# Kernel optimization log

Measured on AMD Instinct MI355X. Metric: run time of the kernel, lower is better.

## Reference

```python
import jax, jax.numpy as jnp
import numpy as np

OVERFLOW_MARGIN = 1e-08

N, D, OUT = 8192, 128, 128


def setup_inputs() -> dict:
    key = jax.random.key(0)
    k1, k2, k3 = jax.random.split(key, 3)
    values = jax.random.normal(k1, (N, D), dtype=jnp.float32)
    adjacency = jax.random.uniform(k2, (N, N), dtype=jnp.float32)
    W = jax.random.normal(k3, (D, OUT), dtype=jnp.float32) * 0.05
    b = jnp.zeros((OUT,), dtype=jnp.float32)
    return {"values": values, "adjacency": adjacency, "W": W, "b": b}


def reference(values, adjacency, W, b):
    # Dense projection: fc_sc = values @ W + b  -> [N, OUT]
    fc_sc = values @ W + b
    # degree d = A @ ones -> row sums, [N]
    d = jnp.sum(adjacency, axis=1)
    d_inv_sqrt = 1.0 / (jnp.sqrt(d) + OVERFLOW_MARGIN)  # [N]
    # laplacian = diag(d_inv_sqrt) @ A @ diag(d_inv_sqrt)
    # expressed as row/col broadcast scaling (same math, no NxN diag matmuls)
    laplacian = adjacency * d_inv_sqrt[:, None] * d_inv_sqrt[None, :]
    # graph conv: [N,N] @ [N,OUT]
    return laplacian @ fc_sc
```

## Files before the change

kernel.cpp:

```cpp
#include <hip/hip_runtime.h>

#define NROWS 8192
#define DIM   128
#define RSTRIDE 136

typedef __attribute__((ext_vector_type(8))) short  short8;
typedef __attribute__((ext_vector_type(4))) float  floatx4;

union frag_u { unsigned u[4]; short8 v; };

__device__ __forceinline__ unsigned pk_bf16(float a, float b) {
  unsigned ua = __float_as_uint(a);
  ua += 0x7fffu + ((ua >> 16) & 1u);
  unsigned ub = __float_as_uint(b);
  ub += 0x7fffu + ((ub >> 16) & 1u);
  return (ua >> 16) | (ub & 0xffff0000u);
}

__global__ __launch_bounds__(256) void k_rowsum(const float* __restrict__ A,
                                                float* __restrict__ s) {
  int row = blockIdx.x;
  const float4* A4 = (const float4*)(A + (size_t)row * NROWS);
  float sum = 0.f;
#pragma unroll
  for (int it = 0; it < NROWS / 4 / 256; ++it) {
    float4 v = A4[threadIdx.x + it * 256];
    sum += (v.x + v.y) + (v.z + v.w);
  }
#pragma unroll
  for (int off = 32; off > 0; off >>= 1) sum += __shfl_down(sum, off, 64);
  __shared__ float red[4];
  int lane = threadIdx.x & 63, w = threadIdx.x >> 6;
  if (lane == 0) red[w] = sum;
  __syncthreads();
  if (threadIdx.x == 0) {
    float d = (red[0] + red[1]) + (red[2] + red[3]);
    s[row] = 1.0f / (sqrtf(d) + 1e-8f);
  }
}

__global__ __launch_bounds__(256) void k_fc(const float* __restrict__ V,
                                            const float* __restrict__ W,
                                            const float* __restrict__ b,
                                            const float* __restrict__ s,
                                            unsigned short* __restrict__ gT) {
  __shared__ float Wl[DIM * DIM];
  __shared__ float Vl[32 * DIM];
  __shared__ unsigned short Fl[32 * DIM];
  int r0 = blockIdx.x * 32;
  {
    const float4* Wg = (const float4*)W;
    float4* Wd = (float4*)Wl;
#pragma unroll
    for (int i = 0; i < DIM * DIM / 4 / 256; ++i)
      Wd[threadIdx.x + i * 256] = Wg[threadIdx.x + i * 256];
    const float4* Vg = (const float4*)(V + (size_t)r0 * DIM);
    float4* Vd = (float4*)Vl;
#pragma unroll
    for (int i = 0; i < 32 * DIM / 4 / 256; ++i)
      Vd[threadIdx.x + i * 256] = Vg[threadIdx.x + i * 256];
  }
  __syncthreads();

  int cg = threadIdx.x & 31;
  int rg = threadIdx.x >> 5;
  float acc[4][4] = {};
  for (int d = 0; d < DIM; ++d) {
    float4 w = *(const float4*)&Wl[d * DIM + cg * 4];
#pragma unroll
    for (int rr = 0; rr < 4; ++rr) {
      float v = Vl[(rg * 4 + rr) * DIM + d];
      acc[rr][0] += v * w.x; acc[rr][1] += v * w.y;
      acc[rr][2] += v * w.z; acc[rr][3] += v * w.w;
    }
  }
  float bb[4], sv[4];
#pragma unroll
  for (int cc = 0; cc < 4; ++cc) bb[cc] = b[cg * 4 + cc];
#pragma unroll
  for (int rr = 0; rr < 4; ++rr) sv[rr] = s[r0 + rg * 4 + rr];
#pragma unroll
  for (int rr = 0; rr < 4; ++rr)
#pragma unroll
    for (int cc = 0; cc < 4; cc += 2) {
      unsigned p = pk_bf16((acc[rr][cc]     + bb[cc])     * sv[rr],
                           (acc[rr][cc + 1] + bb[cc + 1]) * sv[rr]);
      *(unsigned*)&Fl[(rg * 4 + rr) * DIM + cg * 4 + cc] = p;
    }
  __syncthreads();

  int k = threadIdx.x & 127, h = threadIdx.x >> 7;
  unsigned wb[8];
#pragma unroll
  for (int rr = 0; rr < 8; ++rr) {
    unsigned lo = Fl[(h * 16 + 2 * rr) * DIM + k];
    unsigned hi = Fl[(h * 16 + 2 * rr + 1) * DIM + k];
    wb[rr] = lo | (hi << 16);
  }
  uint4* dst = (uint4*)(gT + (size_t)k * NROWS + r0 + h * 16);
  dst[0] = make_uint4(wb[0], wb[1], wb[2], wb[3]);
  dst[1] = make_uint4(wb[4], wb[5], wb[6], wb[7]);
}

__global__ __launch_bounds__(512, 4) void k_spmm(const float* __restrict__ A,
                                                 const unsigned short* __restrict__ gT,
                                                 const float* __restrict__ s,
                                                 float* __restrict__ out) {
  __shared__ float red[8 * 16 * RSTRIDE];
  int tid  = threadIdx.x;
  int w    = tid >> 6, lane = tid & 63;
  int l15  = lane & 15, quad = lane >> 4;
  int i0   = blockIdx.x * 16;
  int j0   = w * (NROWS / 8);

  floatx4 acc[8];
#pragma unroll
  for (int mt = 0; mt < 8; ++mt) acc[mt] = (floatx4){0.f, 0.f, 0.f, 0.f};

  const unsigned short* gp = gT + (size_t)l15 * NROWS + j0 + quad * 8;
  const float*          ap = A + (size_t)(i0 + l15) * NROWS + j0 + quad * 8;

#pragma unroll 2
  for (int jj = 0; jj < NROWS / 8; jj += 32) {
    short8 bfrag;
    {
      float4 lo = *(const float4*)(ap);
      float4 hi = *(const float4*)(ap + 4);
      frag_u f;
      f.u[0] = pk_bf16(lo.x, lo.y); f.u[1] = pk_bf16(lo.z, lo.w);
      f.u[2] = pk_bf16(hi.x, hi.y); f.u[3] = pk_bf16(hi.z, hi.w);
      bfrag = f.v;
    }
    short8 afrag[8];
#pragma unroll
    for (int mt = 0; mt < 8; ++mt)
      afrag[mt] = *(const short8*)(gp + mt * 16 * NROWS);
#pragma unroll
    for (int mt = 0; mt < 8; ++mt)
      acc[mt] = __builtin_amdgcn_mfma_f32_16x16x32_bf16(afrag[mt], bfrag, acc[mt], 0, 0, 0);
    gp += 32; ap += 32;
  }

  float* myred = red + w * 16 * RSTRIDE + l15 * RSTRIDE + quad * 4;
#pragma unroll
  for (int mt = 0; mt < 8; ++mt) {
    float4 v = make_float4(acc[mt][0], acc[mt][1], acc[mt][2], acc[mt][3]);
    *(float4*)(myred + mt * 16) = v;
  }
  __syncthreads();

  int row = tid >> 5;
  int c4  = (tid & 31) * 4;
  float4 sum = make_float4(0.f, 0.f, 0.f, 0.f);
#pragma unroll
  for (int ww = 0; ww < 8; ++ww) {
    float4 v = *(const float4*)(red + ww * 16 * RSTRIDE + row * RSTRIDE + c4);
    sum.x += v.x; sum.y += v.y; sum.z += v.z; sum.w += v.w;
  }
  float si = s[i0 + row];
  sum.x *= si; sum.y *= si; sum.z *= si; sum.w *= si;
  *(float4*)(out + (size_t)(i0 + row) * DIM + c4) = sum;
}

extern "C" void kernel_launch(void* const* d_in, const int* in_sizes, int n_in,
                              void* d_out, int out_size, void* d_ws, size_t ws_size,
                              hipStream_t stream) {
  const float* values    = (const float*)d_in[0];
  const float* adjacency = (const float*)d_in[1];
  const float* W         = (const float*)d_in[2];
  const float* b         = (const float*)d_in[3];
  float* out = (float*)d_out;

  float* s = (float*)d_ws;
  unsigned short* gT = (unsigned short*)((char*)d_ws + 32768);

  k_rowsum<<<NROWS, 256, 0, stream>>>(adjacency, s);
  k_fc<<<NROWS / 32, 256, 0, stream>>>(values, W, b, s, gT);
  k_spmm<<<NROWS / 16, 512, 0, stream>>>(adjacency, gT, s, out);
}
```

Measured before the change: 523.6 us.

## Pre-convert adjacency to tiled bf16 layout and split-K spmm with partial reduction

Fuses the degree row-sum with a pass that converts the adjacency matrix to bf16 in an MFMA-fragment-tiled layout. This lets the spmm kernel issue contiguous fragment loads and skip per-iteration conversion. The projected features are stored in a matching tiled layout, and spmm now computes two row blocks per wave across four K-splits. Partial results go through a separate reduce kernel that applies the row scaling. The change adds an extra 128MB write/read of the bf16 adjacency, atomics for the degree, and more kernel launches.

```diff
diff --git a/kernel.cpp b/kernel.cpp
--- a/kernel.cpp
+++ b/kernel.cpp
@@ -2,12 +2,11 @@
 
 #define NROWS 8192
 #define DIM   128
-#define RSTRIDE 136
+#define RS    132
+#define PSTR  520
 
 typedef __attribute__((ext_vector_type(8))) short  short8;
 typedef __attribute__((ext_vector_type(4))) float  floatx4;
-
-union frag_u { unsigned u[4]; short8 v; };
 
 __device__ __forceinline__ unsigned pk_bf16(float a, float b) {
   unsigned ua = __float_as_uint(a);
@@ -17,33 +16,57 @@
   return (ua >> 16) | (ub & 0xffff0000u);
 }
 
-__global__ __launch_bounds__(256) void k_rowsum(const float* __restrict__ A,
-                                                float* __restrict__ s) {
-  int row = blockIdx.x;
-  const float4* A4 = (const float4*)(A + (size_t)row * NROWS);
+__global__ __launch_bounds__(256) void k_prep(const float* __restrict__ A,
+                                              float* __restrict__ d,
+                                              unsigned short* __restrict__ Abf) {
+  __shared__ unsigned short B[16 * PSTR];
+  __shared__ float rsum[16 * 17];
+  int iblk = blockIdx.x;
+  int wb   = blockIdx.y;
+  int i0   = iblk * 16;
+  int jwin = wb * 512;
+  int t = threadIdx.x;
+  int r = t >> 4, l16 = t & 15;
+
+  const float* ap = A + (size_t)(i0 + r) * NROWS + jwin + l16 * 8;
   float sum = 0.f;
 #pragma unroll
-  for (int it = 0; it < NROWS / 4 / 256; ++it) {
-    float4 v = A4[threadIdx.x + it * 256];
-    sum += (v.x + v.y) + (v.z + v.w);
-  }
-#pragma unroll
-  for (int off = 32; off > 0; off >>= 1) sum += __shfl_down(sum, off, 64);
-  __shared__ float red[4];
-  int lane = threadIdx.x & 63, w = threadIdx.x >> 6;
-  if (lane == 0) red[w] = sum;
-  __syncthreads();
-  if (threadIdx.x == 0) {
-    float d = (red[0] + red[1]) + (red[2] + red[3]);
-    s[row] = 1.0f / (sqrtf(d) + 1e-8f);
-  }
+  for (int it = 0; it < 4; ++it) {
+    float4 lo = *(const float4*)(ap + it * 128);
+    float4 hi = *(const float4*)(ap + it * 128 + 4);
+    sum += (lo.x + lo.y) + (lo.z + lo.w) + (hi.x + hi.y) + (hi.z + hi.w);
+    uint4 p = make_uint4(pk_bf16(lo.x, lo.y), pk_bf16(lo.z, lo.w),
+                         pk_bf16(hi.x, hi.y), pk_bf16(hi.z, hi.w));
+    *(uint4*)&B[r * PSTR + l16 * 8 + it * 128] = p;
+  }
+  rsum[r * 17 + l16] = sum;
+  __syncthreads();
+  if (t < 16) {
+    float s2 = 0.f;
+#pragma unroll
+    for (int c = 0; c < 16; ++c) s2 += rsum[t * 17 + c];
+    atomicAdd(&d[i0 + t], s2);
+  }
+  int jb = t >> 4, p = t & 15;
+  unsigned short* tbase = Abf + ((size_t)iblk * 256 + wb * 16 + jb) * 512;
+#pragma unroll
+  for (int q = 0; q < 4; ++q) {
+    uint4 v = *(const uint4*)&B[p * PSTR + jb * 32 + q * 8];
+    *(uint4*)(tbase + (size_t)(q * 16 + p) * 8) = v;
+  }
+}
+
+__global__ __launch_bounds__(256) void k_sconv(const float* __restrict__ d,
+                                               float* __restrict__ s) {
+  int i = blockIdx.x * 256 + threadIdx.x;
+  s[i] = 1.0f / (sqrtf(d[i]) + 1e-8f);
 }
 
 __global__ __launch_bounds__(256) void k_fc(const float* __restrict__ V,
                                             const float* __restrict__ W,
                                             const float* __restrict__ b,
                                             const float* __restrict__ s,
-                                            unsigned short* __restrict__ gT) {
+                                            unsigned short* __restrict__ gTt) {
   __shared__ float Wl[DIM * DIM];
   __shared__ float Vl[32 * DIM];
   __shared__ unsigned short Fl[32 * DIM];
@@ -65,11 +88,11 @@
   int cg = threadIdx.x & 31;
   int rg = threadIdx.x >> 5;
   float acc[4][4] = {};
-  for (int d = 0; d < DIM; ++d) {
-    float4 w = *(const float4*)&Wl[d * DIM + cg * 4];
+  for (int dd = 0; dd < DIM; ++dd) {
+    float4 w = *(const float4*)&Wl[dd * DIM + cg * 4];
 #pragma unroll
     for (int rr = 0; rr < 4; ++rr) {
-      float v = Vl[(rg * 4 + rr) * DIM + d];
+      float v = Vl[(rg * 4 + rr) * DIM + dd];
       acc[rr][0] += v * w.x; acc[rr][1] += v * w.y;
       acc[rr][2] += v * w.z; acc[rr][3] += v * w.w;
     }
@@ -89,77 +112,100 @@
     }
   __syncthreads();
 
-  int k = threadIdx.x & 127, h = threadIdx.x >> 7;
-  unsigned wb[8];
-#pragma unroll
-  for (int rr = 0; rr < 8; ++rr) {
-    unsigned lo = Fl[(h * 16 + 2 * rr) * DIM + k];
-    unsigned hi = Fl[(h * 16 + 2 * rr + 1) * DIM + k];
-    wb[rr] = lo | (hi << 16);
-  }
-  uint4* dst = (uint4*)(gT + (size_t)k * NROWS + r0 + h * 16);
-  dst[0] = make_uint4(wb[0], wb[1], wb[2], wb[3]);
-  dst[1] = make_uint4(wb[4], wb[5], wb[6], wb[7]);
-}
-
-__global__ __launch_bounds__(512, 4) void k_spmm(const float* __restrict__ A,
-                                                 const unsigned short* __restrict__ gT,
-                                                 const float* __restrict__ s,
-                                                 float* __restrict__ out) {
-  __shared__ float red[8 * 16 * RSTRIDE];
-  int tid  = threadIdx.x;
-  int w    = tid >> 6, lane = tid & 63;
-  int l15  = lane & 15, quad = lane >> 4;
-  int i0   = blockIdx.x * 16;
-  int j0   = w * (NROWS / 8);
-
-  floatx4 acc[8];
-#pragma unroll
-  for (int mt = 0; mt < 8; ++mt) acc[mt] = (floatx4){0.f, 0.f, 0.f, 0.f};
-
-  const unsigned short* gp = gT + (size_t)l15 * NROWS + j0 + quad * 8;
-  const float*          ap = A + (size_t)(i0 + l15) * NROWS + j0 + quad * 8;
+  int kblk = threadIdx.x >> 5, s5 = threadIdx.x & 31;
+  int jblk = r0 >> 5;
+#pragma unroll
+  for (int h = 0; h < 2; ++h) {
+    int L = s5 + h * 32;
+    int l15 = L & 15, quad = L >> 4;
+    int k = kblk * 16 + l15;
+    unsigned w0 = (unsigned)Fl[(quad * 8 + 0) * DIM + k] | ((unsigned)Fl[(quad * 8 + 1) * DIM + k] << 16);
+    unsigned w1 = (unsigned)Fl[(quad * 8 + 2) * DIM + k] | ((unsigned)Fl[(quad * 8 + 3) * DIM + k] << 16);
+    unsigned w2 = (unsigned)Fl[(quad * 8 + 4) * DIM + k] | ((unsigned)Fl[(quad * 8 + 5) * DIM + k] << 16);
+    unsigned w3 = (unsigned)Fl[(quad * 8 + 6) * DIM + k] | ((unsigned)Fl[(quad * 8 + 7) * DIM + k] << 16);
+    *(uint4*)(gTt + ((size_t)(kblk * 256 + jblk) * 64 + L) * 8) = make_uint4(w0, w1, w2, w3);
+  }
+}
+
+__global__ __launch_bounds__(256, 4) void k_spmm(const unsigned short* __restrict__ Abf,
+                                                 const unsigned short* __restrict__ gTt,
+                                                 float* __restrict__ partial) {
+  __shared__ float red[4 * 32 * RS];
+  int t = threadIdx.x, w = t >> 6, lane = t & 63;
+  int bi = blockIdx.x >> 2, ks = blockIdx.x & 3;
+  int jblk0 = ks * 64 + w * 16;
+
+  const unsigned short* ab = Abf + ((size_t)bi * 2 * 256 + jblk0) * 512 + lane * 8;
+  const unsigned short* gb = gTt + (size_t)jblk0 * 512 + lane * 8;
+
+  floatx4 acc[8][2];
+#pragma unroll
+  for (int kb = 0; kb < 8; ++kb)
+#pragma unroll
+    for (int ib = 0; ib < 2; ++ib)
+      acc[kb][ib] = (floatx4){0.f, 0.f, 0.f, 0.f};
 
 #pragma unroll 2
-  for (int jj = 0; jj < NROWS / 8; jj += 32) {
-    short8 bfrag;
-    {
-      float4 lo = *(const float4*)(ap);
-      float4 hi = *(const float4*)(ap + 4);
-      frag_u f;
-      f.u[0] = pk_bf16(lo.x, lo.y); f.u[1] = pk_bf16(lo.z, lo.w);
-      f.u[2] = pk_bf16(hi.x, hi.y); f.u[3] = pk_bf16(hi.z, hi.w);
-      bfrag = f.v;
-    }
-    short8 afrag[8];
-#pragma unroll
-    for (int mt = 0; mt < 8; ++mt)
-      afrag[mt] = *(const short8*)(gp + mt * 16 * NROWS);
-#pragma unroll
-    for (int mt = 0; mt < 8; ++mt)
-      acc[mt] = __builtin_amdgcn_mfma_f32_16x16x32_bf16(afrag[mt], bfrag, acc[mt], 0, 0, 0);
-    gp += 32; ap += 32;
-  }
-
-  float* myred = red + w * 16 * RSTRIDE + l15 * RSTRIDE + quad * 4;
-#pragma unroll
-  for (int mt = 0; mt < 8; ++mt) {
-    float4 v = make_float4(acc[mt][0], acc[mt][1], acc[mt][2], acc[mt][3]);
-    *(float4*)(myred + mt * 16) = v;
-  }
-  __syncthreads();
-
-  int row = tid >> 5;
-  int c4  = (tid & 31) * 4;
-  float4 sum = make_float4(0.f, 0.f, 0.f, 0.f);
-#pragma unroll
-  for (int ww = 0; ww < 8; ++ww) {
-    float4 v = *(const float4*)(red + ww * 16 * RSTRIDE + row * RSTRIDE + c4);
-    sum.x += v.x; sum.y += v.y; sum.z += v.z; sum.w += v.w;
-  }
-  float si = s[i0 + row];
-  sum.x *= si; sum.y *= si; sum.z *= si; sum.w *= si;
-  *(float4*)(out + (size_t)(i0 + row) * DIM + c4) = sum;
+  for (int it = 0; it < 16; ++it) {
+    short8 af0 = *(const short8*)(ab);
+    short8 af1 = *(const short8*)(ab + (size_t)256 * 512);
+    short8 gf[8];
+#pragma unroll
+    for (int kb = 0; kb < 8; ++kb)
+      gf[kb] = *(const short8*)(gb + (size_t)kb * 256 * 512);
+#pragma unroll
+    for (int kb = 0; kb < 8; ++kb) {
+      acc[kb][0] = __builtin_amdgcn_mfma_f32_16x16x32_bf16(gf[kb], af0, acc[kb][0], 0, 0, 0);
+      acc[kb][1] = __builtin_amdgcn_mfma_f32_16x16x32_bf16(gf[kb], af1, acc[kb][1], 0, 0, 0);
+    }
+    ab += 512; gb += 512;
+  }
+
+  int l15 = lane & 15, quad = lane >> 4;
+  float* myred = red + w * 32 * RS;
+#pragma unroll
+  for (int ib = 0; ib < 2; ++ib)
+#pragma unroll
+    for (int kb = 0; kb < 8; ++kb) {
+      float4 v = make_float4(acc[kb][ib][0], acc[kb][ib][1], acc[kb][ib][2], acc[kb][ib][3]);
+      *(float4*)(myred + (ib * 16 + l15) * RS + kb * 16 + quad * 4) = v;
+    }
+  __syncthreads();
+
+  int ii = t >> 3, kg = (t & 7) * 16;
+  float4 sum[4];
+#pragma unroll
+  for (int c = 0; c < 4; ++c) sum[c] = make_float4(0.f, 0.f, 0.f, 0.f);
+#pragma unroll
+  for (int ww = 0; ww < 4; ++ww)
+#pragma unroll
+    for (int c = 0; c < 4; ++c) {
+      float4 v = *(const float4*)(red + ww * 32 * RS + ii * RS + kg + c * 4);
+      sum[c].x += v.x; sum[c].y += v.y; sum[c].z += v.z; sum[c].w += v.w;
+    }
+  float* pout = partial + ((size_t)(ks * 256 + bi) * 32 + ii) * 128 + kg;
+#pragma unroll
+  for (int c = 0; c < 4; ++c) *(float4*)(pout + c * 4) = sum[c];
+}
+
+__global__ __launch_bounds__(256) void k_reduce(const float* __restrict__ partial,
+                                                const float* __restrict__ s,
+                                                float* __restrict__ out) {
+  int g = blockIdx.x * 256 + threadIdx.x;
+  int i = g >> 5, c4 = (g & 31) * 4;
+  size_t base = (size_t)i * 128 + c4;
+  const size_t kstr = (size_t)256 * 32 * 128;
+  float4 a = *(const float4*)(partial + base);
+  float4 bq = *(const float4*)(partial + base + kstr);
+  float4 c = *(const float4*)(partial + base + 2 * kstr);
+  float4 dq = *(const float4*)(partial + base + 3 * kstr);
+  float si = s[i];
+  float4 r;
+  r.x = si * (a.x + bq.x + c.x + dq.x);
+  r.y = si * (a.y + bq.y + c.y + dq.y);
+  r.z = si * (a.z + bq.z + c.z + dq.z);
+  r.w = si * (a.w + bq.w + c.w + dq.w);
+  *(float4*)(out + base) = r;
 }
 
 extern "C" void kernel_launch(void* const* d_in, const int* in_sizes, int n_in,
@@ -171,10 +217,17 @@
   const float* b         = (const float*)d_in[3];
   float* out = (float*)d_out;
 
-  float* s = (float*)d_ws;
-  unsigned short* gT = (unsigned short*)((char*)d_ws + 32768);
-
-  k_rowsum<<<NROWS, 256, 0, stream>>>(adjacency, s);
-  k_fc<<<NROWS / 32, 256, 0, stream>>>(values, W, b, s, gT);
-  k_spmm<<<NROWS / 16, 512, 0, stream>>>(adjacency, gT, s, out);
-}
+  char* ws = (char*)d_ws;
+  float* d            = (float*)ws;
+  float* s            = (float*)(ws + 32768);
+  unsigned short* gTt = (unsigned short*)(ws + 65536);
+  float* partial      = (float*)(ws + 65536 + 2097152);
+  unsigned short* Abf = (unsigned short*)(ws + 33554432);
+
+  hipMemsetAsync(d, 0, NROWS * sizeof(float), stream);
+  k_prep<<<dim3(512, 16), 256, 0, stream>>>(adjacency, d, Abf);
+  k_sconv<<<NROWS / 256, 256, 0, stream>>>(d, s);
+  k_fc<<<NROWS / 32, 256, 0, stream>>>(values, W, b, s, gTt);
+  k_spmm<<<1024, 256, 0, stream>>>(Abf, gTt, partial);
+  k_reduce<<<NROWS * 32 / 256, 256, 0, stream>>>(partial, s, out);
+}
```

After: 449.7 us. 1.16x faster.
